# Performance work log

Hardware: AMD Instinct MI355X
Metric: run time of the kernel (lower is better)

Reference implementation:

```python
import jax, jax.numpy as jnp
import numpy as np

# Sizes
N, E = 100000, 3200000
F_NODE, F_EDGE, LD, HID, L = 4, 4, 6, 16, 8
ALPHA = 1.0
EPS = 1e-6


def setup_inputs() -> dict:
    key = jax.random.key(0)
    ks = jax.random.split(key, 8)
    x = jax.random.normal(ks[0], (N, F_NODE), jnp.float32)
    fixed_mask = jax.random.uniform(ks[1], (N,)) < 0.1
    x = x.at[:, -1].set(jnp.where(fixed_mask, jnp.abs(x[:, -1]) + 1.0, 0.0))
    # positive edge attributes (pipe resistance etc.)
    edge_attr = jax.random.uniform(ks[2], (E, F_EDGE), jnp.float32) * 0.9 + 0.1
    edge_index = jax.random.randint(ks[3], (2, E), 0, N, dtype=jnp.int64)
    d_in = 2 * LD + 2 * F_NODE + F_EDGE  # 24: [x_src, x_dst, attr_src, attr_dst, edge_attr]
    s = 0.1
    W1 = jax.random.normal(ks[4], (L, d_in, HID), jnp.float32) * s
    b1 = jnp.zeros((L, HID), jnp.float32)
    W2 = jax.random.normal(ks[5], (L, HID, LD), jnp.float32) * s
    b2 = jnp.zeros((L, LD), jnp.float32)
    Wf = jax.random.normal(ks[6], (LD, 1), jnp.float32) * s
    bf = jnp.zeros((1,), jnp.float32)
    return {"x": x, "edge_attr": edge_attr, "edge_index": edge_index,
            "W1": W1, "b1": b1, "W2": W2, "b2": b2, "Wf": Wf, "bf": bf}


def reference(x, edge_attr, edge_index, W1, b1, W2, b2, Wf, bf):
    src, dst = edge_index[0], edge_index[1]
    # in-degree for mean aggregation
    deg = jax.ops.segment_sum(jnp.ones((E,), jnp.float32), dst, num_segments=N)
    deg = jnp.maximum(deg, 1.0)
    X = jnp.zeros((N, LD), jnp.float32)
    na_src, na_dst = x[src], x[dst]  # static node-attr gathers reused each layer
    for l in range(L):  # num_convs GNNSConv layers
        m_in = jnp.concatenate([X[src], X[dst], na_src, na_dst, edge_attr], axis=-1)  # [E,24]
        h = jax.nn.relu(m_in @ W1[l] + b1[l])         # per-edge MLP hidden [E,16]
        m = h @ W2[l] + b2[l]                          # per-edge message [E,6]
        agg = jax.ops.segment_sum(m, dst, num_segments=N) / deg[:, None]  # mean aggr
        X = (1.0 - ALPHA) * X + ALPHA * agg            # latent update (alpha_update_x)
        X = jax.nn.relu(X)
    P = jax.nn.relu(X @ Wf + bf)                       # [N,1]
    fixed = x[:, -1]
    P_ = jnp.where(fixed != 0, fixed, P.reshape(-1))   # keep known pressures
    # BalanceConv: gas-network flow from squared-pressure drop, k = edge resistance
    dp2 = P_[src] ** 2 - P_[dst] ** 2
    k = edge_attr[:, 0]
    flows = jnp.sign(dp2) * jnp.sqrt(jnp.abs(dp2) / k + EPS)  # [E]
    inj = x[:, 0]  # nodal injection/demand
    balance = (jax.ops.segment_sum(flows, dst, num_segments=N)
               - jax.ops.segment_sum(flows, src, num_segments=N) + inj)
    imbalance = jnp.sqrt(jnp.sum(balance ** 2))
    return P, flows, jnp.stack([imbalance])
```

## Files before the change

### kernel.cpp

```cpp
#include <hip/hip_runtime.h>
#include <math.h>

#define N_NODES 100000
#define N_EDGES 3200000
#define F_NODE 4
#define F_EDGE 4
#define LD 6
#define HID 16
#define NLAYER 8
#define EPSF 1e-6f

#define NPB 64
#define NBK 1563
#define NBIN 196
#define G1 1000
#define CH (N_EDGES / G1)
#define SPLIT 4
#define NSB (NBIN * SPLIT)

__device__ __forceinline__ unsigned f2bf(float a, float b) {
    unsigned ua = __float_as_uint(a);
    ua = (ua + 0x7fffu + ((ua >> 16) & 1u)) >> 16;
    unsigned ub = __float_as_uint(b);
    ub = (ub + 0x7fffu + ((ub >> 16) & 1u)) & 0xffff0000u;
    return ua | ub;
}
__device__ __forceinline__ float bflo(unsigned u) { return __uint_as_float(u << 16); }
__device__ __forceinline__ float bfhi(unsigned u) { return __uint_as_float(u & 0xffff0000u); }

__global__ __launch_bounds__(256) void hist_kernel(const int* __restrict__ ei,
                                                   int* __restrict__ ghd,
                                                   int* __restrict__ ghs) {
    __shared__ int hd[NBIN];
    __shared__ int hs[NBIN];
    int t = threadIdx.x, blk = blockIdx.x;
    for (int i = t; i < NBIN; i += 256) { hd[i] = 0; hs[i] = 0; }
    __syncthreads();
    int beg = blk * CH, end = beg + CH;
    for (int e = beg + t; e < end; e += 256) {
        atomicAdd(&hs[ei[e] >> 9], 1);
        atomicAdd(&hd[ei[N_EDGES + e] >> 9], 1);
    }
    __syncthreads();
    for (int i = t; i < NBIN; i += 256) {
        ghd[(size_t)i * G1 + blk] = hd[i];
        ghs[(size_t)i * G1 + blk] = hs[i];
    }
}

__global__ __launch_bounds__(256) void scanb_kernel(int* __restrict__ ghd, int* __restrict__ ghs,
                                                    int* __restrict__ totd, int* __restrict__ tots) {
    __shared__ int part[256];
    int b = blockIdx.x, t = threadIdx.x;
#pragma unroll
    for (int a = 0; a < 2; a++) {
        int* g = a ? ghs : ghd;
        int vals[4];
        int sum = 0;
#pragma unroll
        for (int k = 0; k < 4; k++) {
            int idx = t * 4 + k;
            vals[k] = (idx < G1) ? g[(size_t)b * G1 + idx] : 0;
            sum += vals[k];
        }
        part[t] = sum;
        __syncthreads();
        for (int off = 1; off < 256; off <<= 1) {
            int v = (t >= off) ? part[t - off] : 0;
            __syncthreads();
            part[t] += v;
            __syncthreads();
        }
        int excl = part[t] - sum;
#pragma unroll
        for (int k = 0; k < 4; k++) {
            int idx = t * 4 + k;
            if (idx < G1) g[(size_t)b * G1 + idx] = excl;
            excl += vals[k];
        }
        if (t == 0) (a ? tots : totd)[b] = part[255];
        __syncthreads();
    }
}

__global__ __launch_bounds__(256) void totscan_kernel(const int* __restrict__ totd,
                                                      const int* __restrict__ tots,
                                                      int* __restrict__ binbased,
                                                      int* __restrict__ binbases) {
    __shared__ int part[256];
    int t = threadIdx.x;
#pragma unroll
    for (int a = 0; a < 2; a++) {
        const int* tot = a ? tots : totd;
        int* base = a ? binbases : binbased;
        int v = (t < NBIN) ? tot[t] : 0;
        part[t] = v;
        __syncthreads();
        for (int off = 1; off < 256; off <<= 1) {
            int u = (t >= off) ? part[t - off] : 0;
            __syncthreads();
            part[t] += u;
            __syncthreads();
        }
        if (t < NBIN) base[t] = part[t] - v;
        if (t == 0) base[NBIN] = N_EDGES;
        __syncthreads();
    }
}

__global__ __launch_bounds__(256) void scatterA_kernel(const int* __restrict__ ei,
                                                       const float* __restrict__ ea,
                                                       const int* __restrict__ ghd,
                                                       const int* __restrict__ ghs,
                                                       const int* __restrict__ binbased,
                                                       const int* __restrict__ binbases,
                                                       unsigned* __restrict__ aw0,
                                                       unsigned* __restrict__ aw1,
                                                       unsigned* __restrict__ aw2,
                                                       unsigned* __restrict__ sbufA) {
    __shared__ int curd[NBIN];
    __shared__ int curs[NBIN];
    int t = threadIdx.x, blk = blockIdx.x;
    for (int i = t; i < NBIN; i += 256) {
        curd[i] = binbased[i] + ghd[(size_t)i * G1 + blk];
        curs[i] = binbases[i] + ghs[(size_t)i * G1 + blk];
    }
    __syncthreads();
    int beg = blk * CH, end = beg + CH;
    for (int e = beg + t; e < end; e += 256) {
        int s = ei[e], d = ei[N_EDGES + e];
        float4 ev = reinterpret_cast<const float4*>(ea)[e];
        int p = atomicAdd(&curd[d >> 9], 1);
        aw0[p] = (unsigned)s | ((unsigned)(d & 511) << 17);
        aw1[p] = f2bf(ev.x, ev.y);
        aw2[p] = f2bf(ev.z, ev.w);
        int q = atomicAdd(&curs[s >> 9], 1);
        sbufA[q] = (unsigned)e | ((unsigned)(s & 511) << 22);
    }
}

__global__ __launch_bounds__(256) void sr_hist(const unsigned* __restrict__ aw0,
                                               const int* __restrict__ binbased,
                                               int* __restrict__ srh) {
    __shared__ int hist[512];
    int bs = blockIdx.x, t = threadIdx.x;
    int b = bs >> 2, h = bs & 3;
    hist[t] = 0; hist[t + 256] = 0;
    __syncthreads();
    int beg = binbased[b], end = binbased[b + 1];
    int len = end - beg;
    int p0 = beg + (int)((long long)len * h / SPLIT);
    int p1 = beg + (int)((long long)len * (h + 1) / SPLIT);
    for (int i = p0 + t; i < p1; i += 256)
        atomicAdd(&hist[(aw0[i] >> 17) & 511u], 1);
    __syncthreads();
    int* g = srh + (size_t)bs * 512;
    g[t] = hist[t];
    g[t + 256] = hist[t + 256];
}

__global__ __launch_bounds__(256) void sr_scat(const unsigned* __restrict__ aw0,
                                               const unsigned* __restrict__ aw1,
                                               const unsigned* __restrict__ aw2,
                                               const int* __restrict__ binbased,
                                               const int* __restrict__ srh,
                                               unsigned* __restrict__ bw0,
                                               unsigned* __restrict__ bw1,
                                               unsigned* __restrict__ bw2,
                                               float* __restrict__ degInv,
                                               int* __restrict__ based_bk) {
    __shared__ int cur[512];
    __shared__ int part[256];
    int bs = blockIdx.x, t = threadIdx.x;
    int b = bs >> 2, h = bs & 3;
    int beg = binbased[b], end = binbased[b + 1];
    int j0 = 2 * t, j1 = 2 * t + 1;
    int tot0 = 0, tot1 = 0, own0 = 0, own1 = 0;
    const int* gb = srh + (size_t)(b << 2) * 512;
#pragma unroll
    for (int hh = 0; hh < SPLIT; hh++) {
        int v0 = gb[hh * 512 + j0];
        int v1 = gb[hh * 512 + j1];
        if (hh < h) { own0 += v0; own1 += v1; }
        tot0 += v0; tot1 += v1;
    }
    int tsum = tot0 + tot1;
    part[t] = tsum;
    __syncthreads();
    for (int off = 1; off < 256; off <<= 1) {
        int v = (t >= off) ? part[t - off] : 0;
        __syncthreads();
        part[t] += v;
        __syncthreads();
    }
    int excl = part[t] - tsum;
    cur[j0] = beg + excl + own0;
    cur[j1] = beg + excl + tot0 + own1;
    if (h == 0) {
        int node0 = b << 9;
        if (node0 + j0 < N_NODES) degInv[node0 + j0] = 1.0f / fmaxf((float)tot0, 1.0f);
        if (node0 + j1 < N_NODES) degInv[node0 + j1] = 1.0f / fmaxf((float)tot1, 1.0f);
        if ((t & 31) == 0) {
            int k = t >> 5;
            int node = node0 + (k << 6);
            if (node < N_NODES) based_bk[(b << 3) + k] = beg + excl;
        }
        if (b == NBIN - 1 && t == 0) based_bk[NBK] = N_EDGES;
    }
    __syncthreads();
    int len = end - beg;
    int p0 = beg + (int)((long long)len * h / SPLIT);
    int p1 = beg + (int)((long long)len * (h + 1) / SPLIT);
    for (int i = p0 + t; i < p1; i += 256) {
        unsigned r0 = aw0[i];
        int nib = (int)((r0 >> 17) & 511u);
        int p = atomicAdd(&cur[nib], 1);
        bw0[p] = (r0 & 0x1FFFFu) | ((unsigned)(nib & 63) << 17);
        bw1[p] = aw1[i];
        bw2[p] = aw2[i];
    }
}

__global__ __launch_bounds__(256) void ss_hist(const unsigned* __restrict__ sbufA,
                                               const int* __restrict__ binbases,
                                               int* __restrict__ ssh) {
    __shared__ int hist[512];
    int bs = blockIdx.x, t = threadIdx.x;
    int b = bs >> 2, h = bs & 3;
    hist[t] = 0; hist[t + 256] = 0;
    __syncthreads();
    int beg = binbases[b], end = binbases[b + 1];
    int len = end - beg;
    int p0 = beg + (int)((long long)len * h / SPLIT);
    int p1 = beg + (int)((long long)len * (h + 1) / SPLIT);
    for (int i = p0 + t; i < p1; i += 256)
        atomicAdd(&hist[(sbufA[i] >> 22) & 511u], 1);
    __syncthreads();
    int* g = ssh + (size_t)bs * 512;
    g[t] = hist[t];
    g[t + 256] = hist[t + 256];
}

__global__ __launch_bounds__(256) void ss_scat(const unsigned* __restrict__ sbufA,
                                               const int* __restrict__ binbases,
                                               const int* __restrict__ ssh,
                                               unsigned* __restrict__ sbufB,
                                               int* __restrict__ bases_bk) {
    __shared__ int cur[512];
    __shared__ int part[256];
    int bs = blockIdx.x, t = threadIdx.x;
    int b = bs >> 2, h = bs & 3;
    int beg = binbases[b], end = binbases[b + 1];
    int j0 = 2 * t, j1 = 2 * t + 1;
    int tot0 = 0, tot1 = 0, own0 = 0, own1 = 0;
    const int* gb = ssh + (size_t)(b << 2) * 512;
#pragma unroll
    for (int hh = 0; hh < SPLIT; hh++) {
        int v0 = gb[hh * 512 + j0];
        int v1 = gb[hh * 512 + j1];
        if (hh < h) { own0 += v0; own1 += v1; }
        tot0 += v0; tot1 += v1;
    }
    int tsum = tot0 + tot1;
    part[t] = tsum;
    __syncthreads();
    for (int off = 1; off < 256; off <<= 1) {
        int v = (t >= off) ? part[t - off] : 0;
        __syncthreads();
        part[t] += v;
        __syncthreads();
    }
    int excl = part[t] - tsum;
    cur[j0] = beg + excl + own0;
    cur[j1] = beg + excl + tot0 + own1;
    if (h == 0) {
        if ((t & 31) == 0) {
            int k = t >> 5;
            int node = (b << 9) + (k << 6);
            if (node < N_NODES) bases_bk[(b << 3) + k] = beg + excl;
        }
        if (b == NBIN - 1 && t == 0) bases_bk[NBK] = N_EDGES;
    }
    __syncthreads();
    int len = end - beg;
    int p0 = beg + (int)((long long)len * h / SPLIT);
    int p1 = beg + (int)((long long)len * (h + 1) / SPLIT);
    for (int i = p0 + t; i < p1; i += 256) {
        unsigned w = sbufA[i];
        int nib = (int)((w >> 22) & 511u);
        int p = atomicAdd(&cur[nib], 1);
        sbufB[p] = (w & 0x3FFFFFu) | ((unsigned)(nib & 63) << 22);
    }
}

__global__ __launch_bounds__(256) void ab_init(const float* __restrict__ x,
                                               const float* __restrict__ W1,
                                               const float* __restrict__ b1,
                                               unsigned* __restrict__ A,
                                               unsigned* __restrict__ B) {
    __shared__ float sW[8 * HID];
    __shared__ float sb[HID];
    int t = threadIdx.x;
    for (int i = t; i < 8 * HID; i += 256) sW[i] = W1[12 * HID + i];
    if (t < HID) sb[t] = b1[t];
    __syncthreads();
    int i = blockIdx.x * 256 + t;
    if (i >= N_NODES) return;
    float4 xv = reinterpret_cast<const float4*>(x)[i];
    float xf[4] = {xv.x, xv.y, xv.z, xv.w};
    float a[HID], bb[HID];
#pragma unroll
    for (int j = 0; j < HID; j++) { a[j] = sb[j]; bb[j] = 0.0f; }
#pragma unroll
    for (int r = 0; r < 4; r++) {
        float v = xf[r];
#pragma unroll
        for (int j = 0; j < HID; j++) {
            a[j]  = fmaf(v, sW[r * HID + j], a[j]);
            bb[j] = fmaf(v, sW[(4 + r) * HID + j], bb[j]);
        }
    }
    uint4* Ao = reinterpret_cast<uint4*>(A + (size_t)i * 8);
    Ao[0] = make_uint4(f2bf(a[0], a[1]), f2bf(a[2], a[3]), f2bf(a[4], a[5]), f2bf(a[6], a[7]));
    Ao[1] = make_uint4(f2bf(a[8], a[9]), f2bf(a[10], a[11]), f2bf(a[12], a[13]), f2bf(a[14], a[15]));
    uint4* Bo = reinterpret_cast<uint4*>(B + (size_t)i * 8);
    Bo[0] = make_uint4(f2bf(bb[0], bb[1]), f2bf(bb[2], bb[3]), f2bf(bb[4], bb[5]), f2bf(bb[6], bb[7]));
    Bo[1] = make_uint4(f2bf(bb[8], bb[9]), f2bf(bb[10], bb[11]), f2bf(bb[12], bb[13]), f2bf(bb[14], bb[15]));
}

template <int LAST>
__global__ __launch_bounds__(256) void edge_layer(const unsigned* __restrict__ bw0,
                                                  const unsigned* __restrict__ bw1,
                                                  const unsigned* __restrict__ bw2,
                                                  const unsigned* __restrict__ Ain,
                                                  const unsigned* __restrict__ Bin,
                                                  const float* __restrict__ x,
                                                  const float* __restrict__ degInv,
                                                  const float* __restrict__ W1l,
                                                  const float* __restrict__ W2l,
                                                  const float* __restrict__ b2l,
                                                  const float* __restrict__ W1n,
                                                  const float* __restrict__ b1n,
                                                  const float* __restrict__ Wf,
                                                  const float* __restrict__ bfp,
                                                  const int* __restrict__ based_bk,
                                                  unsigned* __restrict__ Aout,
                                                  unsigned* __restrict__ Bout,
                                                  float* __restrict__ Pout,
                                                  float* __restrict__ Pbuf) {
    __shared__ float sWea[4 * HID];
    __shared__ float sW2[HID * LD];
    __shared__ float sb2[LD];
    __shared__ float sW1n[20 * HID];
    __shared__ float sb1n[HID];
    __shared__ float sWf[LD];
    __shared__ float sbf;
    __shared__ float accf[LD * NPB];
    __shared__ unsigned sB[NPB * 8];
    int t = threadIdx.x;
    int b = blockIdx.x;
    for (int i = t; i < 4 * HID; i += 256) sWea[i] = W1l[20 * HID + i];
    for (int i = t; i < HID * LD; i += 256) sW2[i] = W2l[i];
    if (t < LD) sb2[t] = b2l[t];
    if (!LAST) {
        for (int i = t; i < 20 * HID; i += 256) sW1n[i] = W1n[i];
        if (t < HID) sb1n[t] = b1n[t];
    } else {
        if (t < LD) sWf[t] = Wf[t];
        if (t == 0) sbf = bfp[0];
    }
    for (int i = t; i < LD * NPB; i += 256) accf[i] = 0.0f;
    {
        size_t base8 = (size_t)(b << 6) * 8;
        for (int i = t; i < NPB * 8; i += 256) {
            size_t gi = base8 + i;
            sB[i] = (gi < (size_t)N_NODES * 8) ? Bin[gi] : 0u;
        }
    }
    __syncthreads();

    int beg = based_bk[b], end = based_bk[b + 1];
    int lane = t & 63;

    for (int base = beg; base < end; base += 256) {
        int p = base + t;
        bool valid = p < end;
        int key = -1;
        float out[LD];
#pragma unroll
        for (int o = 0; o < LD; o++) out[o] = 0.0f;

        if (valid) {
            unsigned r0 = bw0[p];
            unsigned w1 = bw1[p];
            unsigned w2 = bw2[p];
            int s = (int)(r0 & 0x1FFFFu);
            key = (int)((r0 >> 17) & 63u);
            const uint4* Ap = reinterpret_cast<const uint4*>(Ain + (size_t)s * 8);
            uint4 ax = Ap[0], ay = Ap[1];
            const uint4* Bp = reinterpret_cast<const uint4*>(sB) + key * 2;
            uint4 bx = Bp[0], by = Bp[1];
            float h[HID];
            h[0]  = bflo(ax.x) + bflo(bx.x);  h[1]  = bfhi(ax.x) + bfhi(bx.x);
            h[2]  = bflo(ax.y) + bflo(bx.y);  h[3]  = bfhi(ax.y) + bfhi(bx.y);
            h[4]  = bflo(ax.z) + bflo(bx.z);  h[5]  = bfhi(ax.z) + bfhi(bx.z);
            h[6]  = bflo(ax.w) + bflo(bx.w);  h[7]  = bfhi(ax.w) + bfhi(bx.w);
            h[8]  = bflo(ay.x) + bflo(by.x);  h[9]  = bfhi(ay.x) + bfhi(by.x);
            h[10] = bflo(ay.y) + bflo(by.y);  h[11] = bfhi(ay.y) + bfhi(by.y);
            h[12] = bflo(ay.z) + bflo(by.z);  h[13] = bfhi(ay.z) + bfhi(by.z);
            h[14] = bflo(ay.w) + bflo(by.w);  h[15] = bfhi(ay.w) + bfhi(by.w);
            float ef[4] = {bflo(w1), bfhi(w1), bflo(w2), bfhi(w2)};
#pragma unroll
            for (int rr = 0; rr < 4; rr++) {
                float v = ef[rr];
#pragma unroll
                for (int j = 0; j < HID; j++) h[j] = fmaf(v, sWea[rr * HID + j], h[j]);
            }
#pragma unroll
            for (int j = 0; j < HID; j++) h[j] = fmaxf(h[j], 0.0f);
#pragma unroll
            for (int o = 0; o < LD; o++) out[o] = sb2[o];
#pragma unroll
            for (int j = 0; j < HID; j++) {
                float hj = h[j];
#pragma unroll
                for (int o = 0; o < LD; o++) out[o] = fmaf(hj, sW2[j * LD + o], out[o]);
            }
        }

#pragma unroll
        for (int st = 1; st < 64; st <<= 1) {
            int kup = __shfl_up(key, st, 64);
            bool same = (lane >= st) && (kup == key);
#pragma unroll
            for (int o = 0; o < LD; o++) {
                float v = __shfl_up(out[o], st, 64);
                if (same) out[o] += v;
            }
        }
        int knx = __shfl_down(key, 1, 64);
        bool tail = (lane == 63) || (knx != key);
        if (valid && tail) {
#pragma unroll
            for (int o = 0; o < LD; o++) atomicAdd(&accf[o * NPB + key], out[o]);
        }
    }
    __syncthreads();

    if (t < NPB) {
        int gid = (b << 6) + t;
        if (gid < N_NODES) {
            float inv = degInv[gid];
            float Xv[LD];
#pragma unroll
            for (int o = 0; o < LD; o++) Xv[o] = fmaxf(accf[o * NPB + t] * inv, 0.0f);
            if (LAST) {
                float a2 = sbf;
#pragma unroll
                for (int o = 0; o < LD; o++) a2 = fmaf(Xv[o], sWf[o], a2);
                float P = fmaxf(a2, 0.0f);
                Pout[gid] = P;
                float fx = x[gid * F_NODE + 3];
                Pbuf[gid] = (fx != 0.0f) ? fx : P;
            } else {
                float4 xv = reinterpret_cast<const float4*>(x)[gid];
                float xf[4] = {xv.x, xv.y, xv.z, xv.w};
                float a[HID], bb[HID];
#pragma unroll
                for (int j = 0; j < HID; j++) { a[j] = sb1n[j]; bb[j] = 0.0f; }
#pragma unroll
                for (int rr = 0; rr < LD; rr++) {
                    float v = Xv[rr];
#pragma unroll
                    for (int j = 0; j < HID; j++) {
                        a[j]  = fmaf(v, sW1n[rr * HID + j], a[j]);
                        bb[j] = fmaf(v, sW1n[(LD + rr) * HID + j], bb[j]);
                    }
                }
#pragma unroll
                for (int rr = 0; rr < 4; rr++) {
                    float v = xf[rr];
#pragma unroll
                    for (int j = 0; j < HID; j++) {
                        a[j]  = fmaf(v, sW1n[(12 + rr) * HID + j], a[j]);
                        bb[j] = fmaf(v, sW1n[(16 + rr) * HID + j], bb[j]);
                    }
                }
                uint4* Ao = reinterpret_cast<uint4*>(Aout + (size_t)gid * 8);
                Ao[0] = make_uint4(f2bf(a[0], a[1]), f2bf(a[2], a[3]), f2bf(a[4], a[5]), f2bf(a[6], a[7]));
                Ao[1] = make_uint4(f2bf(a[8], a[9]), f2bf(a[10], a[11]), f2bf(a[12], a[13]), f2bf(a[14], a[15]));
                uint4* Bo = reinterpret_cast<uint4*>(Bout + (size_t)gid * 8);
                Bo[0] = make_uint4(f2bf(bb[0], bb[1]), f2bf(bb[2], bb[3]), f2bf(bb[4], bb[5]), f2bf(bb[6], bb[7]));
                Bo[1] = make_uint4(f2bf(bb[8], bb[9]), f2bf(bb[10], bb[11]), f2bf(bb[12], bb[13]), f2bf(bb[14], bb[15]));
            }
        }
    }
}

__global__ __launch_bounds__(256) void flows_noatomic(const int* __restrict__ ei,
                                                      const float* __restrict__ ea,
                                                      const float* __restrict__ Pbuf,
                                                      float* __restrict__ flows_out) {
    int e = blockIdx.x * 256 + threadIdx.x;
    if (e >= N_EDGES) return;
    int s = ei[e];
    int d = ei[N_EDGES + e];
    float ps = Pbuf[s], pd = Pbuf[d];
    float dp2 = ps * ps - pd * pd;
    float k = ea[(size_t)e * F_EDGE];
    float sg = (dp2 > 0.0f) ? 1.0f : ((dp2 < 0.0f) ? -1.0f : 0.0f);
    flows_out[e] = sg * sqrtf(fabsf(dp2) / k + EPSF);
}

__global__ __launch_bounds__(256) void balance_in(const unsigned* __restrict__ bw0,
                                                  const unsigned* __restrict__ bw1,
                                                  const float* __restrict__ Pbuf,
                                                  const float* __restrict__ x,
                                                  const int* __restrict__ based_bk,
                                                  float* __restrict__ bal) {
    __shared__ float acc[NPB];
    __shared__ float pdl[NPB];
    int t = threadIdx.x;
    int b = blockIdx.x;
    if (t < NPB) {
        acc[t] = 0.0f;
        int gid = (b << 6) + t;
        pdl[t] = (gid < N_NODES) ? Pbuf[gid] : 0.0f;
    }
    __syncthreads();
    int beg = based_bk[b], end = based_bk[b + 1];
    int lane = t & 63;
    for (int base = beg; base < end; base += 256) {
        int p = base + t;
        bool valid = p < end;
        int key = -1;
        float f = 0.0f;
        if (valid) {
            unsigned r0 = bw0[p];
            int s = (int)(r0 & 0x1FFFFu);
            key = (int)((r0 >> 17) & 63u);
            float ps = Pbuf[s];
            float pd = pdl[key];
            float k = bflo(bw1[p]);
            float dp2 = ps * ps - pd * pd;
            float sg = (dp2 > 0.0f) ? 1.0f : ((dp2 < 0.0f) ? -1.0f : 0.0f);
            f = sg * sqrtf(fabsf(dp2) / k + EPSF);
        }
#pragma unroll
        for (int st = 1; st < 64; st <<= 1) {
            int kup = __shfl_up(key, st, 64);
            float v = __shfl_up(f, st, 64);
            if ((lane >= st) && (kup == key)) f += v;
        }
        int knx = __shfl_down(key, 1, 64);
        bool tail = (lane == 63) || (knx != key);
        if (valid && tail) atomicAdd(&acc[key], f);
    }
    __syncthreads();
    if (t < NPB) {
        int gid = (b << 6) + t;
        if (gid < N_NODES) bal[gid] = acc[t] + x[gid * F_NODE + 0];
    }
}

__global__ __launch_bounds__(256) void balance_out(const unsigned* __restrict__ sbufB,
                                                   const float* __restrict__ flows,
                                                   const int* __restrict__ bases_bk,
                                                   const float* __restrict__ bal,
                                                   float* __restrict__ imb2) {
    __shared__ float acc[NPB];
    int t = threadIdx.x;
    if (t < NPB) acc[t] = 0.0f;
    __syncthreads();
    int b = blockIdx.x;
    int beg = bases_bk[b], end = bases_bk[b + 1];
    int lane = t & 63;
    for (int base = beg; base < end; base += 256) {
        int q = base + t;
        bool valid = q < end;
        int key = -1;
        float f = 0.0f;
        if (valid) {
            unsigned u = sbufB[q];
            key = (int)((u >> 22) & 63u);
            f = flows[u & 0x3FFFFFu];
        }
#pragma unroll
        for (int st = 1; st < 64; st <<= 1) {
            int kup = __shfl_up(key, st, 64);
            float v = __shfl_up(f, st, 64);
            if ((lane >= st) && (kup == key)) f += v;
        }
        int knx = __shfl_down(key, 1, 64);
        bool tail = (lane == 63) || (knx != key);
        if (valid && tail) atomicAdd(&acc[key], f);
    }
    __syncthreads();
    if (t < NPB) {
        float v = 0.0f;
        int gid = (b << 6) + t;
        if (gid < N_NODES) {
            float bv = bal[gid] - acc[t];
            v = bv * bv;
        }
#pragma unroll
        for (int off = 32; off > 0; off >>= 1) v += __shfl_down(v, off, 64);
        if (t == 0) atomicAdd(imb2, v);
    }
}

__global__ void fin_kernel(const float* __restrict__ imb2, float* __restrict__ out) {
    out[0] = sqrtf(imb2[0]);
}

extern "C" void kernel_launch(void* const* d_in, const int* in_sizes, int n_in,
                              void* d_out, int out_size, void* d_ws, size_t ws_size,
                              hipStream_t stream) {
    const float* x   = (const float*)d_in[0];
    const float* ea  = (const float*)d_in[1];
    const int*   ei  = (const int*)d_in[2];
    const float* W1  = (const float*)d_in[3];
    const float* b1  = (const float*)d_in[4];
    const float* W2  = (const float*)d_in[5];
    const float* b2  = (const float*)d_in[6];
    const float* Wf  = (const float*)d_in[7];
    const float* bf_ = (const float*)d_in[8];
    float* out = (float*)d_out;

    const size_t N = N_NODES, E = N_EDGES;

    size_t o = 0;
    auto alloc = [&](size_t n) { size_t r = o; o += (n + 3) & ~(size_t)3; return r; };
    size_t o_bw0      = alloc(E);
    size_t o_bw1      = alloc(E);
    size_t o_bw2      = alloc(E);
    size_t o_aw0      = alloc(E);
    size_t o_aw1      = alloc(E);
    size_t o_aw2      = alloc(E);
    size_t o_sbufA    = alloc(E);
    size_t o_ghd      = alloc((size_t)NBIN * G1);
    size_t o_ghs      = alloc((size_t)NBIN * G1);
    size_t o_srh      = alloc((size_t)NSB * 512);
    size_t o_ssh      = alloc((size_t)NSB * 512);
    size_t o_totd     = alloc(NBIN);
    size_t o_tots     = alloc(NBIN);
    size_t o_binbased = alloc(NBIN + 1);
    size_t o_binbases = alloc(NBIN + 1);
    size_t o_basedbk  = alloc(NBK + 1);
    size_t o_basesbk  = alloc(NBK + 1);
    size_t o_degInv   = alloc(N);
    size_t o_A0       = alloc(8 * N);
    size_t o_B0       = alloc(8 * N);
    size_t o_A1       = alloc(8 * N);
    size_t o_B1       = alloc(8 * N);
    size_t o_Pbuf     = alloc(N);
    size_t o_bal      = alloc(N);
    size_t o_imb2     = alloc(16);
    (void)o;

    int* wsi = (int*)d_ws;
    unsigned* bw0      = (unsigned*)(wsi + o_bw0);
    unsigned* bw1      = (unsigned*)(wsi + o_bw1);
    unsigned* bw2      = (unsigned*)(wsi + o_bw2);
    unsigned* aw0      = (unsigned*)(wsi + o_aw0);
    unsigned* aw1      = (unsigned*)(wsi + o_aw1);
    unsigned* aw2      = (unsigned*)(wsi + o_aw2);
    unsigned* sbufA    = (unsigned*)(wsi + o_sbufA);
    unsigned* sbufB    = (unsigned*)(wsi + o_aw0);
    int*      ghd      = wsi + o_ghd;
    int*      ghs      = wsi + o_ghs;
    int*      srh      = wsi + o_srh;
    int*      ssh      = wsi + o_ssh;
    int*      totd     = wsi + o_totd;
    int*      tots     = wsi + o_tots;
    int*      binbased = wsi + o_binbased;
    int*      binbases = wsi + o_binbases;
    int*      based_bk = wsi + o_basedbk;
    int*      bases_bk = wsi + o_basesbk;
    float*    degInv   = (float*)(wsi + o_degInv);
    unsigned* A0       = (unsigned*)(wsi + o_A0);
    unsigned* B0       = (unsigned*)(wsi + o_B0);
    unsigned* A1       = (unsigned*)(wsi + o_A1);
    unsigned* B1       = (unsigned*)(wsi + o_B1);
    float*    Pbuf     = (float*)(wsi + o_Pbuf);
    float*    bal      = (float*)(wsi + o_bal);
    float*    imb2     = (float*)(wsi + o_imb2);

    const int NB = (N_NODES + 255) / 256;
    const int EB = (N_EDGES + 255) / 256;

    hipMemsetAsync(imb2, 0, sizeof(float), stream);

    hist_kernel<<<G1, 256, 0, stream>>>(ei, ghd, ghs);
    scanb_kernel<<<NBIN, 256, 0, stream>>>(ghd, ghs, totd, tots);
    totscan_kernel<<<1, 256, 0, stream>>>(totd, tots, binbased, binbases);
    scatterA_kernel<<<G1, 256, 0, stream>>>(ei, ea, ghd, ghs, binbased, binbases,
                                            aw0, aw1, aw2, sbufA);
    sr_hist<<<NSB, 256, 0, stream>>>(aw0, binbased, srh);
    sr_scat<<<NSB, 256, 0, stream>>>(aw0, aw1, aw2, binbased, srh,
                                     bw0, bw1, bw2, degInv, based_bk);
    ss_hist<<<NSB, 256, 0, stream>>>(sbufA, binbases, ssh);
    ss_scat<<<NSB, 256, 0, stream>>>(sbufA, binbases, ssh, sbufB, bases_bk);

    ab_init<<<NB, 256, 0, stream>>>(x, W1, b1, A0, B0);

    for (int l = 0; l < NLAYER; l++) {
        const unsigned* Ain = (l & 1) ? A1 : A0;
        const unsigned* Bin = (l & 1) ? B1 : B0;
        unsigned* Aout = (l & 1) ? A0 : A1;
        unsigned* Bout = (l & 1) ? B0 : B1;
        const float* W1l = W1 + (size_t)l * 24 * HID;
        const float* W2l = W2 + (size_t)l * HID * LD;
        const float* b2l = b2 + (size_t)l * LD;
        if (l < NLAYER - 1) {
            edge_layer<0><<<NBK, 256, 0, stream>>>(bw0, bw1, bw2, Ain, Bin, x, degInv,
                                                   W1l, W2l, b2l,
                                                   W1 + (size_t)(l + 1) * 24 * HID,
                                                   b1 + (size_t)(l + 1) * HID,
                                                   Wf, bf_, based_bk,
                                                   Aout, Bout, out, Pbuf);
        } else {
            edge_layer<1><<<NBK, 256, 0, stream>>>(bw0, bw1, bw2, Ain, Bin, x, degInv,
                                                   W1l, W2l, b2l,
                                                   W1, b1, Wf, bf_, based_bk,
                                                   Aout, Bout, out, Pbuf);
        }
    }

    flows_noatomic<<<EB, 256, 0, stream>>>(ei, ea, Pbuf, out + N);
    balance_in<<<NBK, 256, 0, stream>>>(bw0, bw1, Pbuf, x, based_bk, bal);
    balance_out<<<NBK, 256, 0, stream>>>(sbufB, out + N, bases_bk, bal, imb2);
    fin_kernel<<<1, 1, 0, stream>>>(imb2, out + (size_t)N + E);
}
```

Baseline: 961.6 us.

## Stage scatter through LDS with local bin sort; widen edge_layer blocks to 512

The scatterA kernel now sorts each chunk's edges by bin in shared memory, using a local histogram and prefix scan, then writes them out in bin-contiguous order. This replaces per-edge global scattered writes with runs that coalesce better. edge_layer is also launched with 512 threads per block instead of 256, so each block processes more edges per loop iteration. In exchange the scatter kernel uses a large amount of LDS (about 51KB) and reads the edge-index array twice, and the 512-thread launch may lower occupancy or raise register pressure. The edge_layer code is only partly shown, so any hard-coded 256 assumptions elsewhere in it could break with the new block size.

```diff
diff --git a/kernel.cpp b/kernel.cpp
--- a/kernel.cpp
+++ b/kernel.cpp
@@ -15,6 +15,7 @@
 #define NBIN 196
 #define G1 1000
 #define CH (N_EDGES / G1)
+#define EPT ((CH + 255) / 256)
 #define SPLIT 4
 #define NSB (NBIN * SPLIT)
 
@@ -118,25 +119,104 @@
                                                        unsigned* __restrict__ aw1,
                                                        unsigned* __restrict__ aw2,
                                                        unsigned* __restrict__ sbufA) {
-    __shared__ int curd[NBIN];
-    __shared__ int curs[NBIN];
+    __shared__ int hcnt[NBIN];
+    __shared__ int cdl[NBIN];
+    __shared__ int gb[NBIN];
+    __shared__ int part[256];
+    __shared__ unsigned st0[CH];
+    __shared__ unsigned st1[CH];
+    __shared__ unsigned st2[CH];
+    __shared__ unsigned stg[CH];
     int t = threadIdx.x, blk = blockIdx.x;
-    for (int i = t; i < NBIN; i += 256) {
-        curd[i] = binbased[i] + ghd[(size_t)i * G1 + blk];
-        curs[i] = binbases[i] + ghs[(size_t)i * G1 + blk];
-    }
-    __syncthreads();
-    int beg = blk * CH, end = beg + CH;
-    for (int e = beg + t; e < end; e += 256) {
-        int s = ei[e], d = ei[N_EDGES + e];
-        float4 ev = reinterpret_cast<const float4*>(ea)[e];
-        int p = atomicAdd(&curd[d >> 9], 1);
-        aw0[p] = (unsigned)s | ((unsigned)(d & 511) << 17);
-        aw1[p] = f2bf(ev.x, ev.y);
-        aw2[p] = f2bf(ev.z, ev.w);
-        int q = atomicAdd(&curs[s >> 9], 1);
-        sbufA[q] = (unsigned)e | ((unsigned)(s & 511) << 22);
-    }
+    int beg = blk * CH;
+    int lidx[EPT];
+
+    for (int i = t; i < NBIN; i += 256) hcnt[i] = 0;
+    __syncthreads();
+    {
+        int k = 0;
+        for (int i = t; i < CH; i += 256, k++)
+            lidx[k] = atomicAdd(&hcnt[ei[N_EDGES + beg + i] >> 9], 1);
+    }
+    __syncthreads();
+    {
+        int own = (t < NBIN) ? hcnt[t] : 0;
+        part[t] = own;
+        __syncthreads();
+        for (int off = 1; off < 256; off <<= 1) {
+            int v = (t >= off) ? part[t - off] : 0;
+            __syncthreads();
+            part[t] += v;
+            __syncthreads();
+        }
+        if (t < NBIN) {
+            cdl[t] = part[t] - own;
+            gb[t] = binbased[t] + ghd[(size_t)t * G1 + blk];
+        }
+    }
+    __syncthreads();
+    {
+        int k = 0;
+        for (int i = t; i < CH; i += 256, k++) {
+            int e = beg + i;
+            int s = ei[e];
+            int d = ei[N_EDGES + e];
+            float4 ev = reinterpret_cast<const float4*>(ea)[e];
+            int bin = d >> 9;
+            int pos = cdl[bin] + lidx[k];
+            st0[pos] = (unsigned)s | ((unsigned)(d & 511) << 17);
+            st1[pos] = f2bf(ev.x, ev.y);
+            st2[pos] = f2bf(ev.z, ev.w);
+            stg[pos] = (unsigned)(gb[bin] + lidx[k]);
+        }
+    }
+    __syncthreads();
+    for (int i = t; i < CH; i += 256) {
+        unsigned g = stg[i];
+        aw0[g] = st0[i];
+        aw1[g] = st1[i];
+        aw2[g] = st2[i];
+    }
+    __syncthreads();
+
+    for (int i = t; i < NBIN; i += 256) hcnt[i] = 0;
+    __syncthreads();
+    {
+        int k = 0;
+        for (int i = t; i < CH; i += 256, k++)
+            lidx[k] = atomicAdd(&hcnt[ei[beg + i] >> 9], 1);
+    }
+    __syncthreads();
+    {
+        int own = (t < NBIN) ? hcnt[t] : 0;
+        part[t] = own;
+        __syncthreads();
+        for (int off = 1; off < 256; off <<= 1) {
+            int v = (t >= off) ? part[t - off] : 0;
+            __syncthreads();
+            part[t] += v;
+            __syncthreads();
+        }
+        if (t < NBIN) {
+            cdl[t] = part[t] - own;
+            gb[t] = binbases[t] + ghs[(size_t)t * G1 + blk];
+        }
+    }
+    __syncthreads();
+    {
+        int k = 0;
+        for (int i = t; i < CH; i += 256, k++) {
+            int e = beg + i;
+            int s = ei[e];
+            int bin = s >> 9;
+            int pos = cdl[bin] + lidx[k];
+            st0[pos] = (unsigned)e | ((unsigned)(s & 511) << 22);
+            stg[pos] = (unsigned)(gb[bin] + lidx[k]);
+        }
+    }
+    __syncthreads();
+    for (int i = t; i < CH; i += 256)
+        sbufA[stg[i]] = st0[i];
 }
 
 __global__ __launch_bounds__(256) void sr_hist(const unsigned* __restrict__ aw0,
@@ -329,7 +409,7 @@
 }
 
 template <int LAST>
-__global__ __launch_bounds__(256) void edge_layer(const unsigned* __restrict__ bw0,
+__global__ __launch_bounds__(512) void edge_layer(const unsigned* __restrict__ bw0,
                                                   const unsigned* __restrict__ bw1,
                                                   const unsigned* __restrict__ bw2,
                                                   const unsigned* __restrict__ Ain,
@@ -359,20 +439,20 @@
     __shared__ unsigned sB[NPB * 8];
     int t = threadIdx.x;
     int b = blockIdx.x;
-    for (int i = t; i < 4 * HID; i += 256) sWea[i] = W1l[20 * HID + i];
-    for (int i = t; i < HID * LD; i += 256) sW2[i] = W2l[i];
+    for (int i = t; i < 4 * HID; i += 512) sWea[i] = W1l[20 * HID + i];
+    for (int i = t; i < HID * LD; i += 512) sW2[i] = W2l[i];
     if (t < LD) sb2[t] = b2l[t];
     if (!LAST) {
-        for (int i = t; i < 20 * HID; i += 256) sW1n[i] = W1n[i];
+        for (int i = t; i < 20 * HID; i += 512) sW1n[i] = W1n[i];
         if (t < HID) sb1n[t] = b1n[t];
     } else {
         if (t < LD) sWf[t] = Wf[t];
         if (t == 0) sbf = bfp[0];
     }
-    for (int i = t; i < LD * NPB; i += 256) accf[i] = 0.0f;
+    for (int i = t; i < LD * NPB; i += 512) accf[i] = 0.0f;
     {
         size_t base8 = (size_t)(b << 6) * 8;
-        for (int i = t; i < NPB * 8; i += 256) {
+        for (int i = t; i < NPB * 8; i += 512) {
             size_t gi = base8 + i;
             sB[i] = (gi < (size_t)N_NODES * 8) ? Bin[gi] : 0u;
         }
@@ -382,7 +462,7 @@
     int beg = based_bk[b], end = based_bk[b + 1];
     int lane = t & 63;
 
-    for (int base = beg; base < end; base += 256) {
+    for (int base = beg; base < end; base += 512) {
         int p = base + t;
         bool valid = p < end;
         int key = -1;
@@ -713,14 +793,14 @@
         const float* W2l = W2 + (size_t)l * HID * LD;
         const float* b2l = b2 + (size_t)l * LD;
         if (l < NLAYER - 1) {
-            edge_layer<0><<<NBK, 256, 0, stream>>>(bw0, bw1, bw2, Ain, Bin, x, degInv,
+            edge_layer<0><<<NBK, 512, 0, stream>>>(bw0, bw1, bw2, Ain, Bin, x, degInv,
                                                    W1l, W2l, b2l,
                                                    W1 + (size_t)(l + 1) * 24 * HID,
                                                    b1 + (size_t)(l + 1) * HID,
                                                    Wf, bf_, based_bk,
                                                    Aout, Bout, out, Pbuf);
         } else {
-            edge_layer<1><<<NBK, 256, 0, stream>>>(bw0, bw1, bw2, Ain, Bin, x, degInv,
+            edge_layer<1><<<NBK, 512, 0, stream>>>(bw0, bw1, bw2, Ain, Bin, x, degInv,
                                                    W1l, W2l, b2l,
                                                    W1, b1, Wf, bf_, based_bk,
                                                    Aout, Bout, out, Pbuf);
```

Measured after the change: 960.0 us. Within noise of the previous version (-0.2%).
